# Kernel tuning notes

Hardware: AMD Instinct MI355X
Metric: run time of the kernel (lower is better)

The kernel has to match this reference:

```python
import jax, jax.numpy as jnp
import numpy as np

D = 2048      # d_hidden
F = 1408      # d_expert (routed)
E = 8         # n_routed_experts
K = 2         # n_experts_per_token
FS = 2816     # shared expert width = d_expert * n_shared_experts
B, S = 2, 1024


def setup_inputs() -> dict:
    key = jax.random.key(0)
    ks = jax.random.split(key, 9)
    sc = 0.02
    return {
        "x": jax.random.normal(ks[0], (B, S, D), dtype=jnp.float32),
        "Wr": jax.random.normal(ks[1], (E, D), dtype=jnp.float32) * sc,   # router Linear(d_hidden, E).weight
        "Wg": jax.random.normal(ks[2], (E, F, D), dtype=jnp.float32) * sc,  # per-expert W_gate.weight [F,D]
        "Wu": jax.random.normal(ks[3], (E, F, D), dtype=jnp.float32) * sc,  # per-expert W_up.weight
        "Wd": jax.random.normal(ks[4], (E, D, F), dtype=jnp.float32) * sc,  # per-expert W_down.weight [D,F]
        "Wsg": jax.random.normal(ks[5], (FS, D), dtype=jnp.float32) * sc,   # shared expert W_gate
        "Wsu": jax.random.normal(ks[6], (FS, D), dtype=jnp.float32) * sc,   # shared expert W_up
        "Wsd": jax.random.normal(ks[7], (D, FS), dtype=jnp.float32) * sc,   # shared expert W_down
    }


def reference(x, Wr, Wg, Wu, Wd, Wsg, Wsu, Wsd):
    silu = jax.nn.silu

    # Shared expert: SwiGLU FFN over all tokens
    sg = silu(jnp.einsum("bsd,fd->bsf", x, Wsg))
    su = jnp.einsum("bsd,fd->bsf", x, Wsu)
    shared_out = jnp.einsum("bsf,df->bsd", sg * su, Wsd)

    # Gating: softmax over expert logits, then top-k (sum-combine is order-invariant)
    logits = jnp.einsum("bsd,ed->bse", x, Wr)
    scores = jax.nn.softmax(logits, axis=-1)
    topk_scores, topk_idx = jax.lax.top_k(scores, K)            # [B,S,K]
    # Dense combine weights [B,S,E]: topk score where selected, else 0
    w_full = jnp.sum(jax.nn.one_hot(topk_idx, E, dtype=x.dtype) * topk_scores[..., None], axis=-2)

    # Routed experts (dense-over-experts equivalent of sorted grouped-GEMM dispatch)
    g = silu(jnp.einsum("bsd,efd->bsef", x, Wg))                # [B,S,E,F]
    u = jnp.einsum("bsd,efd->bsef", x, Wu)
    out_e = jnp.einsum("bsef,edf->bsed", g * u, Wd)             # [B,S,E,D]
    routed_out = jnp.einsum("bsed,bse->bsd", out_e, w_full)

    return routed_out + shared_out
```

## Files before the change

kernel.cpp:

```cpp
#include <hip/hip_runtime.h>
#include <hip/hip_bf16.h>

#define D_HID 2048
#define F_EXP 1408
#define E_NUM 8
#define FS_SH 2816
#define T_TOK 2048

#define O_WSG 0
#define O_WSU 5767168
#define O_WG  11534336
#define O_WU  34603008
#define O_WSD 57671680
#define O_WD  63438848
#define W_TOT 86507520

#define MAXT 24
#define GU_SH_BLK 176
#define GU_GEMM   440
#define GU_CONV   64
#define DN_GRID   512
#define DN_SH_BLK 128

typedef __attribute__((ext_vector_type(8))) short bf16x8;
typedef __attribute__((ext_vector_type(4))) float f32x4;
typedef __attribute__((ext_vector_type(4))) unsigned short u16x4;

#define AS1 __attribute__((address_space(1)))
#define AS3 __attribute__((address_space(3)))

__device__ __forceinline__ unsigned short f2bf(float f){
  unsigned u = __float_as_uint(f);
  u += 0x7fffu + ((u >> 16) & 1u);
  return (unsigned short)(u >> 16);
}

__global__ __launch_bounds__(256) void convert_w_kernel(
    const float* __restrict__ Wsg, const float* __restrict__ Wsu,
    const float* __restrict__ Wg,  const float* __restrict__ Wu,
    unsigned short* __restrict__ dst)
{
  const long e0 = ((long)blockIdx.x * 256 + threadIdx.x) * 8;
  const float* src; long lo;
  if      (e0 < (long)O_WSU){ src = Wsg; lo = e0 - O_WSG; }
  else if (e0 < (long)O_WG ){ src = Wsu; lo = e0 - O_WSU; }
  else if (e0 < (long)O_WU ){ src = Wg;  lo = e0 - O_WG;  }
  else                      { src = Wu;  lo = e0 - O_WU;  }
  const float4 a = ((const float4*)(src + lo))[0];
  const float4 b = ((const float4*)(src + lo))[1];
  u16x4 h0, h1;
  h0[0]=f2bf(a.x); h0[1]=f2bf(a.y); h0[2]=f2bf(a.z); h0[3]=f2bf(a.w);
  h1[0]=f2bf(b.x); h1[1]=f2bf(b.y); h1[2]=f2bf(b.z); h1[3]=f2bf(b.w);
  ((u16x4*)(dst + e0))[0] = h0;
  ((u16x4*)(dst + e0))[1] = h1;
}

__global__ __launch_bounds__(64) void router_kernel(const float* __restrict__ x,
                                                    const float* __restrict__ Wr,
                                                    unsigned short* __restrict__ xb,
                                                    int* __restrict__ topk_e,
                                                    float* __restrict__ topk_w){
  const int t = blockIdx.x;
  const int lane = threadIdx.x;
  const float* xt = x + (size_t)t * D_HID;
  unsigned short* xbt = xb + (size_t)t * D_HID;
  float acc[E_NUM];
  #pragma unroll
  for (int e=0;e<E_NUM;e++) acc[e]=0.f;
  #pragma unroll
  for (int j=0;j<8;j++){
    const int d = j*256 + lane*4;
    const float4 v = *(const float4*)(xt + d);
    u16x4 h;
    h[0]=f2bf(v.x); h[1]=f2bf(v.y); h[2]=f2bf(v.z); h[3]=f2bf(v.w);
    *(u16x4*)(xbt + d) = h;
    #pragma unroll
    for (int e=0;e<E_NUM;e++){
      const float4 w = *(const float4*)(Wr + e*D_HID + d);
      acc[e] += v.x*w.x + v.y*w.y + v.z*w.z + v.w*w.w;
    }
  }
  #pragma unroll
  for (int e=0;e<E_NUM;e++){
    #pragma unroll
    for (int off=32; off>0; off>>=1) acc[e] += __shfl_xor(acc[e], off);
  }
  if (lane==0){
    float m = acc[0];
    #pragma unroll
    for (int e=1;e<E_NUM;e++) m = fmaxf(m, acc[e]);
    float p[E_NUM]; float s = 0.f;
    #pragma unroll
    for (int e=0;e<E_NUM;e++){ p[e] = expf(acc[e]-m); s += p[e]; }
    const float inv = 1.f/s;
    int i0=0; float b0=p[0];
    #pragma unroll
    for (int e=1;e<E_NUM;e++) if (p[e] > b0){ b0=p[e]; i0=e; }
    int i1=-1; float b1=-1.f;
    #pragma unroll
    for (int e=0;e<E_NUM;e++) if (e!=i0 && p[e] > b1){ b1=p[e]; i1=e; }
    topk_e[t*2+0]=i0; topk_e[t*2+1]=i1;
    topk_w[t*2+0]=b0*inv; topk_w[t*2+1]=b1*inv;
  }
}

__global__ __launch_bounds__(1024) void build_lists_kernel(
    const int* __restrict__ topk_e, const float* __restrict__ topk_w,
    int* __restrict__ cnt, int* __restrict__ offs,
    int* __restrict__ assign_token, float* __restrict__ assign_w,
    int* __restrict__ token_slot,
    int* __restrict__ tile_rowbase, int* __restrict__ tile_e,
    int* __restrict__ tile_valid, int* __restrict__ n_rt)
{
  const int tid  = threadIdx.x;
  const int lane = tid & 63;
  const int wv   = tid >> 6;
  __shared__ int wsum[E_NUM][16];
  __shared__ int tot_s[E_NUM];
  __shared__ int offs_s[E_NUM];

  int   e_loc[4];
  float w_loc[4];
  #pragma unroll
  for (int j=0;j<4;j++){ e_loc[j]=topk_e[tid*4+j]; w_loc[j]=topk_w[tid*4+j]; }

  int c[E_NUM];
  #pragma unroll
  for (int e=0;e<E_NUM;e++){
    int s = 0;
    #pragma unroll
    for (int j=0;j<4;j++) s += (e_loc[j]==e) ? 1 : 0;
    c[e] = s;
  }
  int pre[E_NUM];
  #pragma unroll
  for (int e=0;e<E_NUM;e++){
    int v = c[e];
    #pragma unroll
    for (int off=1; off<64; off<<=1){
      int t = __shfl_up(v, off);
      if (lane >= off) v += t;
    }
    if (lane==63) wsum[e][wv] = v;
    pre[e] = v - c[e];
  }
  __syncthreads();
  if (tid < E_NUM){
    int s = 0;
    #pragma unroll
    for (int w=0; w<16; w++){ int t = wsum[tid][w]; wsum[tid][w] = s; s += t; }
    tot_s[tid] = s;
    cnt[tid]   = s;
  }
  __syncthreads();
  if (tid == 0){
    int s = 0;
    #pragma unroll
    for (int e=0;e<E_NUM;e++){ offs_s[e] = s; offs[e] = s; s += tot_s[e]; }
    int ntl = 0;
    for (int e=0;e<E_NUM;e++){
      for (int r=0; r<tot_s[e]; r+=256){
        tile_rowbase[ntl] = offs_s[e] + r;
        tile_e[ntl]       = e;
        int v = tot_s[e] - r; if (v > 256) v = 256;
        tile_valid[ntl]   = v;
        ntl++;
      }
    }
    n_rt[0] = ntl;
    for (int i=ntl;i<MAXT;i++){ tile_rowbase[i]=0; tile_e[i]=0; tile_valid[i]=0; }
  }
  __syncthreads();
  int local[E_NUM];
  #pragma unroll
  for (int e=0;e<E_NUM;e++) local[e]=0;
  #pragma unroll
  for (int j=0;j<4;j++){
    const int e = e_loc[j];
    int pos = 0;
    #pragma unroll
    for (int ee=0; ee<E_NUM; ee++)
      if (e == ee) pos = offs_s[ee] + wsum[ee][wv] + pre[ee] + local[ee];
    #pragma unroll
    for (int ee=0; ee<E_NUM; ee++) local[ee] += (e == ee) ? 1 : 0;
    const int entry = tid*4 + j;
    assign_token[pos] = entry >> 1;
    assign_w[pos]     = w_loc[j];
    token_slot[entry] = pos;
  }
}

__global__ __launch_bounds__(512,1) void gateup_fused(
    const unsigned short* __restrict__ xb,
    unsigned short* __restrict__ wb,
    const float* __restrict__ Wsd_f, const float* __restrict__ Wd_f,
    unsigned short* __restrict__ h_shared,
    unsigned short* __restrict__ h_routed,
    const int* __restrict__ tile_rowbase, const int* __restrict__ tile_e,
    const int* __restrict__ tile_valid, const int* __restrict__ n_rt,
    const int* __restrict__ assign_token)
{
  __shared__ __align__(16) char As[2][256*128];
  __shared__ __align__(16) char Bg[2][128*128];
  __shared__ __align__(16) char Bu[2][128*128];

  const int tid  = threadIdx.x;
  const int braw = blockIdx.x;

  if (braw >= GU_GEMM){
    const int cb = braw - GU_GEMM;
    const long nchunk = (long)(W_TOT - O_WSD) / 8;
    for (long i = (long)cb*512 + tid; i < nchunk; i += (long)GU_CONV*512){
      const long e0 = (long)O_WSD + i * 8;
      const float* src; long lo;
      if (e0 < (long)O_WD){ src = Wsd_f; lo = e0 - O_WSD; } else { src = Wd_f; lo = e0 - O_WD; }
      const float4 va = ((const float4*)(src + lo))[0];
      const float4 vb = ((const float4*)(src + lo))[1];
      u16x4 h0, h1;
      h0[0]=f2bf(va.x); h0[1]=f2bf(va.y); h0[2]=f2bf(va.z); h0[3]=f2bf(va.w);
      h1[0]=f2bf(vb.x); h1[1]=f2bf(vb.y); h1[2]=f2bf(vb.z); h1[3]=f2bf(vb.w);
      ((u16x4*)(wb + e0))[0] = h0;
      ((u16x4*)(wb + e0))[1] = h1;
    }
    return;
  }

  const int b = (braw % 8) * (GU_GEMM/8) + braw / 8;

  const int lane = tid & 63;
  const int wave = tid >> 6;
  const int wr = wave >> 1;
  const int wc = wave & 1;

  int nt, rowbase, valid, gather;
  const unsigned short *wg_base, *wu_base;
  unsigned short* H; int N;
  if (b < GU_SH_BLK){
    nt = b >> 3; const int mtile = b & 7;
    rowbase = mtile*256; valid = 256; gather = 0;
    wg_base = wb + O_WSG + (size_t)(nt*128) * D_HID;
    wu_base = wb + O_WSU + (size_t)(nt*128) * D_HID;
    H = h_shared; N = FS_SH;
  } else {
    const int rb = b - GU_SH_BLK;
    const int tile = rb % MAXT;
    nt = rb / MAXT;
    if (tile >= n_rt[0]) return;
    rowbase = tile_rowbase[tile];
    valid   = tile_valid[tile];
    const int e = tile_e[tile];
    gather = 1;
    wg_base = wb + O_WG + ((size_t)e*F_EXP + nt*128) * D_HID;
    wu_base = wb + O_WU + ((size_t)e*F_EXP + nt*128) * D_HID;
    H = h_routed; N = F_EXP;
  }

  f32x4 accg[4][4], accu[4][4];
  const f32x4 z = {0.f,0.f,0.f,0.f};
  #pragma unroll
  for (int m=0;m<4;m++)
    #pragma unroll
    for (int n=0;n<4;n++){ accg[m][n]=z; accu[m][n]=z; }

  const char* asrc[4];
  const int rowmax = rowbase + valid - 1;
  const int srccol = ((lane&7)<<4) ^ ((lane>>3)<<4);
  #pragma unroll
  for (int p=0;p<4;p++){
    const int row = wave*32 + p*8 + (lane>>3);
    int idx = rowbase + row;
    if (idx > rowmax) idx = rowmax;
    const size_t grow = gather ? (size_t)assign_token[idx] : (size_t)idx;
    asrc[p] = (const char*)(xb + grow * (size_t)D_HID) + srccol;
  }
  const int brow0 = wave*16 + (lane>>3);
  const char* gsrc = (const char*)(wg_base + (size_t)brow0 * D_HID) + srccol;
  const char* usrc = (const char*)(wu_base + (size_t)brow0 * D_HID) + srccol;
  const int pstrB = 8 * D_HID * 2;

  auto stage = [&](int bi, int kt){
    #pragma unroll
    for (int p=0;p<4;p++){
      __builtin_amdgcn_global_load_lds(
        (const AS1 void*)(asrc[p] + kt*128),
        (AS3 void*)(&As[bi][(wave*4 + p)*1024]), 16, 0, 0);
    }
    #pragma unroll
    for (int p=0;p<2;p++){
      __builtin_amdgcn_global_load_lds(
        (const AS1 void*)(gsrc + p*pstrB + kt*128),
        (AS3 void*)(&Bg[bi][(wave*2 + p)*1024]), 16, 0, 0);
      __builtin_amdgcn_global_load_lds(
        (const AS1 void*)(usrc + p*pstrB + kt*128),
        (AS3 void*)(&Bu[bi][(wave*2 + p)*1024]), 16, 0, 0);
    }
  };

  const int nK = D_HID / 64;
  stage(0, 0);
  int cur = 0;
  for (int kt = 0; kt < nK; ++kt){
    if (kt + 1 < nK){
      stage(cur^1, kt+1);
      asm volatile("s_waitcnt vmcnt(8)\n\ts_barrier" ::: "memory");
    } else {
      asm volatile("s_waitcnt vmcnt(0)\n\ts_barrier" ::: "memory");
    }
    #pragma unroll
    for (int kk=0;kk<2;kk++){
      const int kb = kk*64 + ((lane >> 4) << 4);
      bf16x8 a[4], bg[4], bu[4];
      #pragma unroll
      for (int m=0;m<4;m++){
        const int r = wr*64 + m*16 + (lane & 15);
        a[m] = *(const bf16x8*)(&As[cur][r*128 + (kb ^ ((r & 7) << 4))]);
      }
      #pragma unroll
      for (int n=0;n<4;n++){
        const int r = wc*64 + n*16 + (lane & 15);
        const int ofs = r*128 + (kb ^ ((r & 7) << 4));
        bg[n] = *(const bf16x8*)(&Bg[cur][ofs]);
        bu[n] = *(const bf16x8*)(&Bu[cur][ofs]);
      }
      #pragma unroll
      for (int m=0;m<4;m++)
        #pragma unroll
        for (int n=0;n<4;n++){
          accg[m][n] = __builtin_amdgcn_mfma_f32_16x16x32_bf16(a[m], bg[n], accg[m][n], 0,0,0);
          accu[m][n] = __builtin_amdgcn_mfma_f32_16x16x32_bf16(a[m], bu[n], accu[m][n], 0,0,0);
        }
    }
    asm volatile("s_barrier" ::: "memory");
    cur ^= 1;
  }

  const int colbase = nt*128 + wc*64;
  #pragma unroll
  for (int m=0;m<4;m++){
    #pragma unroll
    for (int r=0;r<4;r++){
      const int rr = wr*64 + m*16 + ((lane >> 4) << 2) + r;
      if (rr < valid){
        unsigned short* orow = H + (size_t)(rowbase + rr) * N;
        #pragma unroll
        for (int n=0;n<4;n++){
          const int col = colbase + n*16 + (lane & 15);
          const float g = accg[m][n][r];
          const float u = accu[m][n][r];
          const float h = (g / (1.f + __expf(-g))) * u;
          orow[col] = f2bf(h);
        }
      }
    }
  }
}

__global__ __launch_bounds__(512,1) void down_fused(
    const unsigned short* __restrict__ h_shared,
    const unsigned short* __restrict__ h_routed,
    const unsigned short* __restrict__ wb,
    float* __restrict__ out, float* __restrict__ y_routed,
    const int* __restrict__ tile_rowbase, const int* __restrict__ tile_e,
    const int* __restrict__ tile_valid, const int* __restrict__ n_rt,
    const float* __restrict__ assign_w)
{
  __shared__ __align__(16) char As[2][256*128];
  __shared__ __align__(16) char Bs[2][128*128];

  const int tid  = threadIdx.x;
  const int braw = blockIdx.x;
  const int b = (braw % 8) * (DN_GRID/8) + braw / 8;
  const int lane = tid & 63;
  const int wave = tid >> 6;
  const int wr = wave >> 1, wc = wave & 1;

  int nt, rowbase, valid, weighted, K;
  const unsigned short *A, *w_base;
  float* Out;
  if (b < DN_SH_BLK){
    nt = b >> 3; const int mtile = b & 7;
    rowbase = mtile*256; valid = 256; weighted = 0;
    A = h_shared; K = FS_SH;
    w_base = wb + O_WSD + (size_t)(nt*128) * FS_SH;
    Out = out;
  } else {
    const int rb = b - DN_SH_BLK;
    const int tile = rb % MAXT;
    nt = rb / MAXT;
    if (tile >= n_rt[0]) return;
    rowbase = tile_rowbase[tile];
    valid   = tile_valid[tile];
    const int e = tile_e[tile];
    weighted = 1;
    A = h_routed; K = F_EXP;
    w_base = wb + O_WD + ((size_t)e*D_HID + nt*128) * F_EXP;
    Out = y_routed;
  }
  const size_t K2 = (size_t)K * 2;

  f32x4 acc[4][4];
  const f32x4 z = {0.f,0.f,0.f,0.f};
  #pragma unroll
  for (int m=0;m<4;m++)
    #pragma unroll
    for (int n=0;n<4;n++) acc[m][n]=z;

  const char* asrc[4];
  const int rowmax = rowbase + valid - 1;
  const int srccol = ((lane&7)<<4) ^ ((lane>>3)<<4);
  #pragma unroll
  for (int p=0;p<4;p++){
    const int row = wave*32 + p*8 + (lane>>3);
    int idx = rowbase + row;
    if (idx > rowmax) idx = rowmax;
    asrc[p] = (const char*)A + (size_t)idx * K2 + srccol;
  }
  const int brow0 = wave*16 + (lane>>3);
  const char* bsrc = (const char*)w_base + (size_t)brow0 * K2 + srccol;
  const size_t pstrB = 8 * K2;

  auto stage = [&](int bi, int kt){
    #pragma unroll
    for (int p=0;p<4;p++){
      __builtin_amdgcn_global_load_lds(
        (const AS1 void*)(asrc[p] + kt*128),
        (AS3 void*)(&As[bi][(wave*4 + p)*1024]), 16, 0, 0);
    }
    #pragma unroll
    for (int p=0;p<2;p++){
      __builtin_amdgcn_global_load_lds(
        (const AS1 void*)(bsrc + p*pstrB + kt*128),
        (AS3 void*)(&Bs[bi][(wave*2 + p)*1024]), 16, 0, 0);
    }
  };

  const int nK = K / 64;
  stage(0, 0);
  int cur = 0;
  for (int kt = 0; kt < nK; ++kt){
    if (kt + 1 < nK){
      stage(cur^1, kt+1);
      asm volatile("s_waitcnt vmcnt(6)\n\ts_barrier" ::: "memory");
    } else {
      asm volatile("s_waitcnt vmcnt(0)\n\ts_barrier" ::: "memory");
    }
    #pragma unroll
    for (int kk=0;kk<2;kk++){
      const int kb = kk*64 + ((lane >> 4) << 4);
      bf16x8 a[4], bb[4];
      #pragma unroll
      for (int m=0;m<4;m++){
        const int r = wr*64 + m*16 + (lane & 15);
        a[m] = *(const bf16x8*)(&As[cur][r*128 + (kb ^ ((r & 7) << 4))]);
      }
      #pragma unroll
      for (int n=0;n<4;n++){
        const int r = wc*64 + n*16 + (lane & 15);
        bb[n] = *(const bf16x8*)(&Bs[cur][r*128 + (kb ^ ((r & 7) << 4))]);
      }
      #pragma unroll
      for (int m=0;m<4;m++)
        #pragma unroll
        for (int n=0;n<4;n++)
          acc[m][n] = __builtin_amdgcn_mfma_f32_16x16x32_bf16(a[m], bb[n], acc[m][n], 0,0,0);
    }
    asm volatile("s_barrier" ::: "memory");
    cur ^= 1;
  }

  const int colbase = nt*128 + wc*64;
  #pragma unroll
  for (int m=0;m<4;m++){
    #pragma unroll
    for (int r=0;r<4;r++){
      const int rr = wr*64 + m*16 + ((lane >> 4) << 2) + r;
      if (rr < valid){
        float w = 1.f;
        if (weighted) w = assign_w[rowbase + rr];
        float* orow = Out + (size_t)(rowbase + rr) * D_HID;
        #pragma unroll
        for (int n=0;n<4;n++){
          const int col = colbase + n*16 + (lane & 15);
          orow[col] = acc[m][n][r] * w;
        }
      }
    }
  }
}

__global__ void combine_kernel(float* __restrict__ out, const float* __restrict__ y,
                               const int* __restrict__ token_slot){
  const int i  = blockIdx.x * blockDim.x + threadIdx.x;
  const int t  = i >> 9;
  const int r4 = i & 511;
  const int s0 = token_slot[t*2+0];
  const int s1 = token_slot[t*2+1];
  const float4 a = ((const float4*)(y + (size_t)s0 * D_HID))[r4];
  const float4 b = ((const float4*)(y + (size_t)s1 * D_HID))[r4];
  float4 o = ((float4*)out)[i];
  o.x += a.x + b.x; o.y += a.y + b.y; o.z += a.z + b.z; o.w += a.w + b.w;
  ((float4*)out)[i] = o;
}

extern "C" void kernel_launch(void* const* d_in, const int* in_sizes, int n_in,
                              void* d_out, int out_size, void* d_ws, size_t ws_size,
                              hipStream_t stream){
  const float* x   = (const float*)d_in[0];
  const float* Wr  = (const float*)d_in[1];
  const float* Wg  = (const float*)d_in[2];
  const float* Wu  = (const float*)d_in[3];
  const float* Wd  = (const float*)d_in[4];
  const float* Wsg = (const float*)d_in[5];
  const float* Wsu = (const float*)d_in[6];
  const float* Wsd = (const float*)d_in[7];
  float* out = (float*)d_out;
  (void)in_sizes; (void)n_in; (void)out_size; (void)ws_size;

  char* ws = (char*)d_ws;
  size_t off = 0;
  auto alloc = [&](size_t bytes)->char*{
    char* p = ws + off; off += (bytes + 255) & ~(size_t)255; return p;
  };

  unsigned short* wb       = (unsigned short*)alloc((size_t)W_TOT * 2);
  unsigned short* xb       = (unsigned short*)alloc((size_t)T_TOK * D_HID * 2);
  unsigned short* h_shared = (unsigned short*)alloc((size_t)T_TOK * FS_SH * 2);
  unsigned short* h_routed = (unsigned short*)alloc((size_t)T_TOK * 2 * F_EXP * 2);
  float*          y_routed = (float*)alloc((size_t)T_TOK * 2 * D_HID * 4);
  int*   topk_e       = (int*)alloc(T_TOK*2*sizeof(int));
  float* topk_w       = (float*)alloc(T_TOK*2*sizeof(float));
  int*   cnt          = (int*)alloc(E_NUM*sizeof(int));
  int*   offs         = (int*)alloc(E_NUM*sizeof(int));
  int*   assign_token = (int*)alloc(T_TOK*2*sizeof(int));
  float* assign_w     = (float*)alloc(T_TOK*2*sizeof(float));
  int*   token_slot   = (int*)alloc(T_TOK*2*sizeof(int));
  int*   tile_rowbase = (int*)alloc(MAXT*sizeof(int));
  int*   tile_e       = (int*)alloc(MAXT*sizeof(int));
  int*   tile_valid   = (int*)alloc(MAXT*sizeof(int));
  int*   n_rt         = (int*)alloc(sizeof(int));

  router_kernel<<<T_TOK, 64, 0, stream>>>(x, Wr, xb, topk_e, topk_w);
  build_lists_kernel<<<1, 1024, 0, stream>>>(topk_e, topk_w, cnt, offs,
      assign_token, assign_w, token_slot, tile_rowbase, tile_e, tile_valid, n_rt);
  convert_w_kernel<<<O_WSD/8/256, 256, 0, stream>>>(Wsg, Wsu, Wg, Wu, wb);

  gateup_fused<<<GU_GEMM + GU_CONV, 512, 0, stream>>>(
      xb, wb, Wsd, Wd, h_shared, h_routed, tile_rowbase, tile_e, tile_valid, n_rt, assign_token);
  down_fused<<<DN_GRID, 512, 0, stream>>>(
      h_shared, h_routed, wb, out, y_routed, tile_rowbase, tile_e, tile_valid, n_rt, assign_w);

  combine_kernel<<<(T_TOK*D_HID/4)/256, 256, 0, stream>>>(out, y_routed, token_slot);
}
```

Measured before the change: 388.1 us.

## Deepen GEMM pipelines to 4-stage K=32 and fuse weight conversion into router

Both GEMM kernels move from a double-buffered K=64 tile loop to a four-buffer ring with K=32 tiles. Three stages are prefetched ahead, so there is one barrier per iteration instead of two, and the LDS swizzle is rewritten for 64-byte rows. Separately, conversion of the gate/up weights to bf16 is merged into the router kernel as extra blocks, which removes one launch and lets conversion overlap with routing. The trade is a smaller K per barrier with more loop iterations, plus 64-thread blocks doing the strided conversion work.

Result: slower. 443.4 us (+14.2%).

```diff
diff --git a/kernel.cpp b/kernel.cpp
--- a/kernel.cpp
+++ b/kernel.cpp
@@ -21,6 +21,7 @@
 #define GU_CONV   64
 #define DN_GRID   512
 #define DN_SH_BLK 128
+#define RT_CONV   512
 
 typedef __attribute__((ext_vector_type(8))) short bf16x8;
 typedef __attribute__((ext_vector_type(4))) float f32x4;
@@ -35,33 +36,36 @@
   return (unsigned short)(u >> 16);
 }
 
-__global__ __launch_bounds__(256) void convert_w_kernel(
+__global__ __launch_bounds__(64) void router_conv_kernel(
+    const float* __restrict__ x,  const float* __restrict__ Wr,
     const float* __restrict__ Wsg, const float* __restrict__ Wsu,
     const float* __restrict__ Wg,  const float* __restrict__ Wu,
-    unsigned short* __restrict__ dst)
+    unsigned short* __restrict__ xb, unsigned short* __restrict__ wb,
+    int* __restrict__ topk_e, float* __restrict__ topk_w)
 {
-  const long e0 = ((long)blockIdx.x * 256 + threadIdx.x) * 8;
-  const float* src; long lo;
-  if      (e0 < (long)O_WSU){ src = Wsg; lo = e0 - O_WSG; }
-  else if (e0 < (long)O_WG ){ src = Wsu; lo = e0 - O_WSU; }
-  else if (e0 < (long)O_WU ){ src = Wg;  lo = e0 - O_WG;  }
-  else                      { src = Wu;  lo = e0 - O_WU;  }
-  const float4 a = ((const float4*)(src + lo))[0];
-  const float4 b = ((const float4*)(src + lo))[1];
-  u16x4 h0, h1;
-  h0[0]=f2bf(a.x); h0[1]=f2bf(a.y); h0[2]=f2bf(a.z); h0[3]=f2bf(a.w);
-  h1[0]=f2bf(b.x); h1[1]=f2bf(b.y); h1[2]=f2bf(b.z); h1[3]=f2bf(b.w);
-  ((u16x4*)(dst + e0))[0] = h0;
-  ((u16x4*)(dst + e0))[1] = h1;
-}
-
-__global__ __launch_bounds__(64) void router_kernel(const float* __restrict__ x,
-                                                    const float* __restrict__ Wr,
-                                                    unsigned short* __restrict__ xb,
-                                                    int* __restrict__ topk_e,
-                                                    float* __restrict__ topk_w){
-  const int t = blockIdx.x;
+  const int b = blockIdx.x;
   const int lane = threadIdx.x;
+  if (b >= T_TOK){
+    const int cb = b - T_TOK;
+    const long nchunk = (long)O_WSD / 8;
+    for (long i = (long)cb*64 + lane; i < nchunk; i += (long)RT_CONV*64){
+      const long e0 = i * 8;
+      const float* src; long lo;
+      if      (e0 < (long)O_WSU){ src = Wsg; lo = e0; }
+      else if (e0 < (long)O_WG ){ src = Wsu; lo = e0 - O_WSU; }
+      else if (e0 < (long)O_WU ){ src = Wg;  lo = e0 - O_WG;  }
+      else                      { src = Wu;  lo = e0 - O_WU;  }
+      const float4 va = ((const float4*)(src + lo))[0];
+      const float4 vb = ((const float4*)(src + lo))[1];
+      u16x4 h0, h1;
+      h0[0]=f2bf(va.x); h0[1]=f2bf(va.y); h0[2]=f2bf(va.z); h0[3]=f2bf(va.w);
+      h1[0]=f2bf(vb.x); h1[1]=f2bf(vb.y); h1[2]=f2bf(vb.z); h1[3]=f2bf(vb.w);
+      ((u16x4*)(wb + e0))[0] = h0;
+      ((u16x4*)(wb + e0))[1] = h1;
+    }
+    return;
+  }
+  const int t = b;
   const float* xt = x + (size_t)t * D_HID;
   unsigned short* xbt = xb + (size_t)t * D_HID;
   float acc[E_NUM];
@@ -200,9 +204,9 @@
     const int* __restrict__ tile_valid, const int* __restrict__ n_rt,
     const int* __restrict__ assign_token)
 {
-  __shared__ __align__(16) char As[2][256*128];
-  __shared__ __align__(16) char Bg[2][128*128];
-  __shared__ __align__(16) char Bu[2][128*128];
+  __shared__ __align__(16) char As[4][256*64];
+  __shared__ __align__(16) char Bg[4][128*64];
+  __shared__ __align__(16) char Bu[4][128*64];
 
   const int tid  = threadIdx.x;
   const int braw = blockIdx.x;
@@ -262,76 +266,71 @@
     #pragma unroll
     for (int n=0;n<4;n++){ accg[m][n]=z; accu[m][n]=z; }
 
-  const char* asrc[4];
+  const char* asrc[2];
   const int rowmax = rowbase + valid - 1;
-  const int srccol = ((lane&7)<<4) ^ ((lane>>3)<<4);
-  #pragma unroll
-  for (int p=0;p<4;p++){
-    const int row = wave*32 + p*8 + (lane>>3);
+  #pragma unroll
+  for (int p=0;p<2;p++){
+    const int c = p*512 + tid;
+    const int row = c >> 2, slot = c & 3;
+    const int col16 = slot ^ ((row>>1)&3);
     int idx = rowbase + row;
     if (idx > rowmax) idx = rowmax;
     const size_t grow = gather ? (size_t)assign_token[idx] : (size_t)idx;
-    asrc[p] = (const char*)(xb + grow * (size_t)D_HID) + srccol;
-  }
-  const int brow0 = wave*16 + (lane>>3);
-  const char* gsrc = (const char*)(wg_base + (size_t)brow0 * D_HID) + srccol;
-  const char* usrc = (const char*)(wu_base + (size_t)brow0 * D_HID) + srccol;
-  const int pstrB = 8 * D_HID * 2;
+    asrc[p] = (const char*)(xb + grow * (size_t)D_HID) + (col16<<4);
+  }
+  const int brw = tid >> 2, bsl = tid & 3;
+  const int bcol16 = bsl ^ ((brw>>1)&3);
+  const char* gsrc = (const char*)(wg_base + (size_t)brw * D_HID) + (bcol16<<4);
+  const char* usrc = (const char*)(wu_base + (size_t)brw * D_HID) + (bcol16<<4);
 
   auto stage = [&](int bi, int kt){
     #pragma unroll
-    for (int p=0;p<4;p++){
+    for (int p=0;p<2;p++)
       __builtin_amdgcn_global_load_lds(
-        (const AS1 void*)(asrc[p] + kt*128),
-        (AS3 void*)(&As[bi][(wave*4 + p)*1024]), 16, 0, 0);
-    }
-    #pragma unroll
-    for (int p=0;p<2;p++){
-      __builtin_amdgcn_global_load_lds(
-        (const AS1 void*)(gsrc + p*pstrB + kt*128),
-        (AS3 void*)(&Bg[bi][(wave*2 + p)*1024]), 16, 0, 0);
-      __builtin_amdgcn_global_load_lds(
-        (const AS1 void*)(usrc + p*pstrB + kt*128),
-        (AS3 void*)(&Bu[bi][(wave*2 + p)*1024]), 16, 0, 0);
-    }
+        (const AS1 void*)(asrc[p] + kt*64),
+        (AS3 void*)(&As[bi][(p*512 + tid)*16]), 16, 0, 0);
+    __builtin_amdgcn_global_load_lds(
+        (const AS1 void*)(gsrc + kt*64),
+        (AS3 void*)(&Bg[bi][tid*16]), 16, 0, 0);
+    __builtin_amdgcn_global_load_lds(
+        (const AS1 void*)(usrc + kt*64),
+        (AS3 void*)(&Bu[bi][tid*16]), 16, 0, 0);
   };
 
-  const int nK = D_HID / 64;
-  stage(0, 0);
-  int cur = 0;
+  const int nK = D_HID / 32;
+  stage(0,0); stage(1,1); stage(2,2);
+
+  const int arow0 = wr*64 + (lane & 15);
+  const int brow0 = wc*64 + (lane & 15);
+  const int sread = (lane >> 4) << 4;
+
+  #pragma unroll 1
   for (int kt = 0; kt < nK; ++kt){
-    if (kt + 1 < nK){
-      stage(cur^1, kt+1);
-      asm volatile("s_waitcnt vmcnt(8)\n\ts_barrier" ::: "memory");
-    } else {
-      asm volatile("s_waitcnt vmcnt(0)\n\ts_barrier" ::: "memory");
-    }
-    #pragma unroll
-    for (int kk=0;kk<2;kk++){
-      const int kb = kk*64 + ((lane >> 4) << 4);
-      bf16x8 a[4], bg[4], bu[4];
-      #pragma unroll
-      for (int m=0;m<4;m++){
-        const int r = wr*64 + m*16 + (lane & 15);
-        a[m] = *(const bf16x8*)(&As[cur][r*128 + (kb ^ ((r & 7) << 4))]);
-      }
+    if (kt < nK-2)       asm volatile("s_waitcnt vmcnt(8)\n\ts_barrier" ::: "memory");
+    else if (kt == nK-2) asm volatile("s_waitcnt vmcnt(4)\n\ts_barrier" ::: "memory");
+    else                 asm volatile("s_waitcnt vmcnt(0)\n\ts_barrier" ::: "memory");
+    const int bi = kt & 3;
+    bf16x8 a[4], bgr[4], bur[4];
+    #pragma unroll
+    for (int m=0;m<4;m++){
+      const int r = arow0 + m*16;
+      a[m] = *(const bf16x8*)(&As[bi][r*64 + (sread ^ (((r>>1)&3)<<4))]);
+    }
+    #pragma unroll
+    for (int n=0;n<4;n++){
+      const int r = brow0 + n*16;
+      const int ofs = r*64 + (sread ^ (((r>>1)&3)<<4));
+      bgr[n] = *(const bf16x8*)(&Bg[bi][ofs]);
+      bur[n] = *(const bf16x8*)(&Bu[bi][ofs]);
+    }
+    if (kt + 3 < nK) stage((kt+3)&3, kt+3);
+    #pragma unroll
+    for (int m=0;m<4;m++)
       #pragma unroll
       for (int n=0;n<4;n++){
-        const int r = wc*64 + n*16 + (lane & 15);
-        const int ofs = r*128 + (kb ^ ((r & 7) << 4));
-        bg[n] = *(const bf16x8*)(&Bg[cur][ofs]);
-        bu[n] = *(const bf16x8*)(&Bu[cur][ofs]);
+        accg[m][n] = __builtin_amdgcn_mfma_f32_16x16x32_bf16(a[m], bgr[n], accg[m][n], 0,0,0);
+        accu[m][n] = __builtin_amdgcn_mfma_f32_16x16x32_bf16(a[m], bur[n], accu[m][n], 0,0,0);
       }
-      #pragma unroll
-      for (int m=0;m<4;m++)
-        #pragma unroll
-        for (int n=0;n<4;n++){
-          accg[m][n] = __builtin_amdgcn_mfma_f32_16x16x32_bf16(a[m], bg[n], accg[m][n], 0,0,0);
-          accu[m][n] = __builtin_amdgcn_mfma_f32_16x16x32_bf16(a[m], bu[n], accu[m][n], 0,0,0);
-        }
-    }
-    asm volatile("s_barrier" ::: "memory");
-    cur ^= 1;
   }
 
   const int colbase = nt*128 + wc*64;
@@ -364,8 +363,8 @@
     const int* __restrict__ tile_valid, const int* __restrict__ n_rt,
     const float* __restrict__ assign_w)
 {
-  __shared__ __align__(16) char As[2][256*128];
-  __shared__ __align__(16) char Bs[2][128*128];
+  __shared__ __align__(16) char As[4][256*64];
+  __shared__ __align__(16) char Bs[4][128*64];
 
   const int tid  = threadIdx.x;
   const int braw = blockIdx.x;
@@ -405,67 +404,62 @@
     #pragma unroll
     for (int n=0;n<4;n++) acc[m][n]=z;
 
-  const char* asrc[4];
+  const char* asrc[2];
   const int rowmax = rowbase + valid - 1;
-  const int srccol = ((lane&7)<<4) ^ ((lane>>3)<<4);
-  #pragma unroll
-  for (int p=0;p<4;p++){
-    const int row = wave*32 + p*8 + (lane>>3);
+  #pragma unroll
+  for (int p=0;p<2;p++){
+    const int c = p*512 + tid;
+    const int row = c >> 2, slot = c & 3;
+    const int col16 = slot ^ ((row>>1)&3);
     int idx = rowbase + row;
     if (idx > rowmax) idx = rowmax;
-    asrc[p] = (const char*)A + (size_t)idx * K2 + srccol;
-  }
-  const int brow0 = wave*16 + (lane>>3);
-  const char* bsrc = (const char*)w_base + (size_t)brow0 * K2 + srccol;
-  const size_t pstrB = 8 * K2;
+    asrc[p] = (const char*)A + (size_t)idx * K2 + (col16<<4);
+  }
+  const int brw = tid >> 2, bsl = tid & 3;
+  const int bcol16 = bsl ^ ((brw>>1)&3);
+  const char* bsrc = (const char*)w_base + (size_t)brw * K2 + (bcol16<<4);
 
   auto stage = [&](int bi, int kt){
     #pragma unroll
-    for (int p=0;p<4;p++){
+    for (int p=0;p<2;p++)
       __builtin_amdgcn_global_load_lds(
-        (const AS1 void*)(asrc[p] + kt*128),
-        (AS3 void*)(&As[bi][(wave*4 + p)*1024]), 16, 0, 0);
-    }
-    #pragma unroll
-    for (int p=0;p<2;p++){
-      __builtin_amdgcn_global_load_lds(
-        (const AS1 void*)(bsrc + p*pstrB + kt*128),
-        (AS3 void*)(&Bs[bi][(wave*2 + p)*1024]), 16, 0, 0);
-    }
+        (const AS1 void*)(asrc[p] + kt*64),
+        (AS3 void*)(&As[bi][(p*512 + tid)*16]), 16, 0, 0);
+    __builtin_amdgcn_global_load_lds(
+        (const AS1 void*)(bsrc + kt*64),
+        (AS3 void*)(&Bs[bi][tid*16]), 16, 0, 0);
   };
 
-  const int nK = K / 64;
-  stage(0, 0);
-  int cur = 0;
+  const int nK = K / 32;
+  stage(0,0); stage(1,1); stage(2,2);
+
+  const int arow0 = wr*64 + (lane & 15);
+  const int brow0 = wc*64 + (lane & 15);
+  const int sread = (lane >> 4) << 4;
+
+  #pragma unroll 1
   for (int kt = 0; kt < nK; ++kt){
-    if (kt + 1 < nK){
-      stage(cur^1, kt+1);
-      asm volatile("s_waitcnt vmcnt(6)\n\ts_barrier" ::: "memory");
-    } else {
-      asm volatile("s_waitcnt vmcnt(0)\n\ts_barrier" ::: "memory");
-    }
-    #pragma unroll
-    for (int kk=0;kk<2;kk++){
-      const int kb = kk*64 + ((lane >> 4) << 4);
-      bf16x8 a[4], bb[4];
+    if (kt < nK-2)       asm volatile("s_waitcnt vmcnt(6)\n\ts_barrier" ::: "memory");
+    else if (kt == nK-2) asm volatile("s_waitcnt vmcnt(3)\n\ts_barrier" ::: "memory");
+    else                 asm volatile("s_waitcnt vmcnt(0)\n\ts_barrier" ::: "memory");
+    const int bi = kt & 3;
+    bf16x8 a[4], bb[4];
+    #pragma unroll
+    for (int m=0;m<4;m++){
+      const int r = arow0 + m*16;
+      a[m] = *(const bf16x8*)(&As[bi][r*64 + (sread ^ (((r>>1)&3)<<4))]);
+    }
+    #pragma unroll
+    for (int n=0;n<4;n++){
+      const int r = brow0 + n*16;
+      bb[n] = *(const bf16x8*)(&Bs[bi][r*64 + (sread ^ (((r>>1)&3)<<4))]);
+    }
+    if (kt + 3 < nK) stage((kt+3)&3, kt+3);
+    #pragma unroll
+    for (int m=0;m<4;m++)
       #pragma unroll
-      for (int m=0;m<4;m++){
-        const int r = wr*64 + m*16 + (lane & 15);
-        a[m] = *(const bf16x8*)(&As[cur][r*128 + (kb ^ ((r & 7) << 4))]);
-      }
-      #pragma unroll
-      for (int n=0;n<4;n++){
-        const int r = wc*64 + n*16 + (lane & 15);
-        bb[n] = *(const bf16x8*)(&Bs[cur][r*128 + (kb ^ ((r & 7) << 4))]);
-      }
-      #pragma unroll
-      for (int m=0;m<4;m++)
-        #pragma unroll
-        for (int n=0;n<4;n++)
-          acc[m][n] = __builtin_amdgcn_mfma_f32_16x16x32_bf16(a[m], bb[n], acc[m][n], 0,0,0);
-    }
-    asm volatile("s_barrier" ::: "memory");
-    cur ^= 1;
+      for (int n=0;n<4;n++)
+        acc[m][n] = __builtin_amdgcn_mfma_f32_16x16x32_bf16(a[m], bb[n], acc[m][n], 0,0,0);
   }
 
   const int colbase = nt*128 + wc*64;
@@ -539,10 +533,10 @@
   int*   tile_valid   = (int*)alloc(MAXT*sizeof(int));
   int*   n_rt         = (int*)alloc(sizeof(int));
 
-  router_kernel<<<T_TOK, 64, 0, stream>>>(x, Wr, xb, topk_e, topk_w);
+  router_conv_kernel<<<T_TOK + RT_CONV, 64, 0, stream>>>(
+      x, Wr, Wsg, Wsu, Wg, Wu, xb, wb, topk_e, topk_w);
   build_lists_kernel<<<1, 1024, 0, stream>>>(topk_e, topk_w, cnt, offs,
       assign_token, assign_w, token_slot, tile_rowbase, tile_e, tile_valid, n_rt);
-  convert_w_kernel<<<O_WSD/8/256, 256, 0, stream>>>(Wsg, Wsu, Wg, Wu, wb);
 
   gateup_fused<<<GU_GEMM + GU_CONV, 512, 0, stream>>>(
       xb, wb, Wsd, Wd, h_shared, h_routed, tile_rowbase, tile_e, tile_valid, n_rt, assign_token);
```
